# Performance work log

Measured on AMD Instinct MI355X. Metric: run time of the kernel, lower is better.

## Reference

```python
import jax, jax.numpy as jnp
import numpy as np

B, D = 8192, 128          # batch, input_dim (one graph node per feature)
ENC1, ENC2 = 256, 128     # encoder hidden dims (encoder_l = 3)
DEC1, DEC2 = 64, 32       # GCN decoder feature dims (decoder_l = 2)
THRESH = 0.1              # adjacency threshold after iter > 50


def setup_inputs():
    key = jax.random.key(0)
    ks = jax.random.split(key, 10)
    f32 = jnp.float32

    def w(k, shape, scale=0.05):
        return jax.random.normal(k, shape, f32) * scale

    return {
        "x": jax.random.normal(ks[0], (B, D), f32),
        "eps": jax.random.normal(ks[1], (B, D), f32),
        "W_enc1": w(ks[2], (D, ENC1)), "b_enc1": jnp.zeros((ENC1,), f32),
        "W_enc2": w(ks[3], (ENC1, ENC2)), "b_enc2": jnp.zeros((ENC2,), f32),
        "W_mu": w(ks[4], (ENC2, D)), "b_mu": jnp.zeros((D,), f32),
        "W_lv": w(ks[5], (ENC2, D)), "b_lv": jnp.zeros((D,), f32),
        "graph_logits": jax.random.normal(ks[6], (D, D), f32),
        "W_feat": w(ks[7], (1, DEC1), 0.1),
        "W_g1": w(ks[8], (DEC1, DEC2)), "b_g1": jnp.zeros((DEC2,), f32),
        "W_g2": w(ks[9], (DEC2, 1)), "b_g2": jnp.zeros((1,), f32),
        "it": 100,
    }


def _learned_graph(graph_logits, it):
    g = jax.nn.sigmoid(graph_logits)
    eye = jnp.eye(g.shape[0], dtype=g.dtype)
    g = g * (1.0 - eye) + eye                 # force self-loops to weight 1
    if it > 50:                               # static python int -> plain if
        g = jnp.where(g < THRESH, jnp.zeros_like(g), g)
    return g


def _gcn(adj, h, W, b):
    # DGL GraphConv norm='both' with edge weights on a batch of identical
    # D-node graphs (block-diagonal batching done densely per-sample):
    #   h' = D_in^{-1/2} (A_w)^T D_out^{-1/2} h W + b
    mask = (adj > 0).astype(h.dtype)
    d_out = jnp.maximum(mask.sum(axis=1), 1.0)
    d_in = jnp.maximum(mask.sum(axis=0), 1.0)
    a_hat = adj * jax.lax.rsqrt(d_out)[:, None] * jax.lax.rsqrt(d_in)[None, :]
    msg = jnp.einsum("ij,bif->bjf", a_hat, h)  # aggregate src->dst over all batch graphs
    return msg @ W + b


def reference(x, eps, W_enc1, b_enc1, W_enc2, b_enc2, W_mu, b_mu, W_lv, b_lv,
              graph_logits, W_feat, W_g1, b_g1, W_g2, b_g2, it):
    # --- VAE encoder + reparameterize ---
    h = jax.nn.relu(x @ W_enc1 + b_enc1)
    h = jax.nn.relu(h @ W_enc2 + b_enc2)
    mu_z = h @ W_mu + b_mu
    logvar_z = h @ W_lv + b_lv
    z = mu_z + eps * jnp.exp(0.5 * logvar_z)   # (B, D)
    # --- learned adjacency over features ---
    adj = _learned_graph(graph_logits, it)     # (D, D)
    # --- graph input processor: each feature -> one node, embed its scalar ---
    hn = z[:, :, None] * W_feat[0]             # (B, D, DEC1)
    # --- homogeneous GCN decoder ---
    hn = jnp.tanh(_gcn(adj, hn, W_g1, b_g1))   # (B, D, DEC2)
    hn = _gcn(adj, hn, W_g2, b_g2)             # (B, D, 1)
    x_hat = hn.reshape(x.shape[0], -1)         # (B, D)
    return (x_hat, adj, mu_z, logvar_z)
```

## Files before the change

### kernel.cpp

```cpp
#include <hip/hip_runtime.h>
#include <math.h>

#define BATCH 8192
#define DIM   128
#define E1    256
#define E2    128

#define OUT_XHAT 0
#define OUT_ADJ  (BATCH*DIM)
#define OUT_MU   (OUT_ADJ + DIM*DIM)
#define OUT_LV   (OUT_MU + BATCH*DIM)

#define W1F   0u
#define W2F   65536u
#define WMUF  131072u
#define WLVF  163840u
#define AHF   196608u
#define COEF  229376u
#define VBUF  229408u

typedef __attribute__((ext_vector_type(8))) short s8v;
typedef __attribute__((ext_vector_type(4))) float f4v;
#define MFMA(a, b, c) __builtin_amdgcn_mfma_f32_16x16x32_bf16(a, b, c, 0, 0, 0)

__device__ __forceinline__ ushort f2bf(float f) {
    uint u = __float_as_uint(f);
    u += 0x7fffu + ((u >> 16) & 1u);
    return (ushort)(u >> 16);
}

__global__ __launch_bounds__(512) void prep_kernel(
    const float* __restrict__ W1,  const float* __restrict__ W2,
    const float* __restrict__ Wmu, const float* __restrict__ Wlv,
    const float* __restrict__ logits, const float* __restrict__ Wf,
    const float* __restrict__ Wg1, const float* __restrict__ bg1,
    const float* __restrict__ Wg2, const int* __restrict__ itp,
    float* __restrict__ out, char* __restrict__ wsb)
{
    __shared__ float gsm[16384];
    __shared__ float aux[768];
    __shared__ float vsh[32];
    const int t = threadIdx.x;

    if (blockIdx.x < 24) {
        const int tid = (int)blockIdx.x * 512 + t;
        const float* W; ushort* dst; int e, N_, ksLog;
        if (tid < 4096)       { W = W1;  dst = (ushort*)(wsb + W1F);  e = tid * 8;           N_ = 256; ksLog = 2; }
        else if (tid < 8192)  { W = W2;  dst = (ushort*)(wsb + W2F);  e = (tid - 4096) * 8;  N_ = 128; ksLog = 3; }
        else if (tid < 10240) { W = Wmu; dst = (ushort*)(wsb + WMUF); e = (tid - 8192) * 8;  N_ = 128; ksLog = 2; }
        else                  { W = Wlv; dst = (ushort*)(wsb + WLVF); e = (tid - 10240) * 8; N_ = 128; ksLog = 2; }
        const int frag = e >> 9, l = (e >> 3) & 63;
        const int nt = frag >> ksLog, ks = frag & ((1 << ksLog) - 1);
        const int k0 = ks * 32 + ((l >> 4) << 3);
        const int n  = (nt << 4) + (l & 15);
        uint pk[4];
        #pragma unroll
        for (int jj = 0; jj < 4; ++jj) {
            ushort lo = f2bf(W[(k0 + 2 * jj) * N_ + n]);
            ushort hi = f2bf(W[(k0 + 2 * jj + 1) * N_ + n]);
            pk[jj] = (uint)lo | ((uint)hi << 16);
        }
        *(uint4*)(dst + e) = make_uint4(pk[0], pk[1], pk[2], pk[3]);
        return;
    }

    const int it = itp[0];
    {
        const int j = t & 127, rq = t >> 7;
        float dp = 0.0f;
        for (int i = rq * 32; i < rq * 32 + 32; ++i) {
            float l = logits[i * DIM + j];
            float gv = 1.0f / (1.0f + expf(-l));
            if (i == j) gv = 1.0f;
            if (it > 50 && gv < 0.1f) gv = 0.0f;
            gsm[i * DIM + j] = gv;
            if (gv > 0.0f) dp += 1.0f;
        }
        aux[rq * 128 + j] = dp;
    }
    __syncthreads();
    if (t < 128) {
        float d = aux[t] + aux[128 + t] + aux[256 + t] + aux[384 + t];
        aux[512 + t] = 1.0f / sqrtf(fmaxf(d, 1.0f));
    }
    __syncthreads();
    {
        const int i = t & 127, cq = t >> 7;
        float dp = 0.0f;
        for (int c = cq * 32; c < cq * 32 + 32; ++c)
            if (gsm[i * DIM + c] > 0.0f) dp += 1.0f;
        aux[cq * 128 + i] = dp;
    }
    __syncthreads();
    if (t < 128) {
        float d = aux[t] + aux[128 + t] + aux[256 + t] + aux[384 + t];
        aux[640 + t] = 1.0f / sqrtf(fmaxf(d, 1.0f));
    }
    __syncthreads();
    for (int p = 0; p < 32; ++p) {
        int idx = t + 512 * p;
        int i = idx >> 7, j = idx & 127;
        float gv = gsm[idx];
        out[OUT_ADJ + idx] = gv;
        gsm[idx] = gv * aux[640 + i] * aux[512 + j];
    }
    if (t < 32) {
        float acc = 0.0f;
        for (int k = 0; k < 64; ++k) acc = fmaf(Wf[k], Wg1[k * 32 + t], acc);
        vsh[t] = acc;
        float* vb = (float*)(wsb + VBUF);
        vb[t] = acc; vb[32 + t] = bg1[t]; vb[64 + t] = Wg2[t];
    }
    __syncthreads();
    {
        ushort* ahf = (ushort*)(wsb + AHF);
        #pragma unroll
        for (int c = 0; c < 4; ++c) {
            int e = (t + c * 512) * 8;
            int frag = e >> 9, l = (e >> 3) & 63;
            int nt = frag >> 2, ks = frag & 3;
            int k0 = ks * 32 + ((l >> 4) << 3);
            int n  = (nt << 4) + (l & 15);
            uint pk[4];
            #pragma unroll
            for (int jj = 0; jj < 4; ++jj) {
                ushort lo = f2bf(gsm[(k0 + 2 * jj) * DIM + n]);
                ushort hi = f2bf(gsm[(k0 + 2 * jj + 1) * DIM + n]);
                pk[jj] = (uint)lo | ((uint)hi << 16);
            }
            *(uint4*)(ahf + e) = make_uint4(pk[0], pk[1], pk[2], pk[3]);
        }
    }
    if (t == 0) {
        float a1 = 0, a3 = 0, a5 = 0, vmax = 0, bmax = 0;
        for (int c = 0; c < 32; ++c) {
            float v = vsh[c], w = Wg2[c], v2 = v * v;
            a1 += w * v;
            a3 -= w * v * v2 * (1.0f / 3.0f);
            a5 += w * v * v2 * v2 * (2.0f / 15.0f);
            vmax = fmaxf(vmax, fabsf(v));
            bmax = fmaxf(bmax, fabsf(bg1[c]));
        }
        float* cf = (float*)(wsb + COEF);
        cf[0] = a1; cf[1] = a3; cf[2] = a5;
        cf[3] = (bmax == 0.0f) ? 0.2f / fmaxf(vmax, 1e-30f) : -1.0f;
    }
}

__global__ __launch_bounds__(256, 2) void fused_kernel(
    const float* __restrict__ x,   const float* __restrict__ eps,
    const float* __restrict__ b1,  const float* __restrict__ b2,
    const float* __restrict__ bmu, const float* __restrict__ blv,
    const float* __restrict__ bg2p,
    float* __restrict__ out, char* __restrict__ wsb)
{
    __shared__ __attribute__((aligned(16))) ushort bufA[2048];
    __shared__ __attribute__((aligned(16))) ushort bufB[4096];
    __shared__ __attribute__((aligned(16))) ushort bufC[2048];
    __shared__ float vls[96];

    const int t = threadIdx.x;
    const int lane = t & 63, wid = t >> 6;
    const int fr = lane & 15, fq = lane >> 4;
    const int row0 = (int)blockIdx.x * 16;

    if (t < 96) vls[t] = ((const float*)(wsb + VBUF))[t];

    {
        const int r = t & 15, g = (t >> 4) & 3, ks = t >> 6;
        const float* src = x + (size_t)(row0 + r) * DIM + ks * 32 + g * 8;
        float4 u0 = *(const float4*)src;
        float4 u1 = *(const float4*)(src + 4);
        uint p0 = (uint)f2bf(u0.x) | ((uint)f2bf(u0.y) << 16);
        uint p1 = (uint)f2bf(u0.z) | ((uint)f2bf(u0.w) << 16);
        uint p2 = (uint)f2bf(u1.x) | ((uint)f2bf(u1.y) << 16);
        uint p3 = (uint)f2bf(u1.z) | ((uint)f2bf(u1.w) << 16);
        *(uint4*)&bufA[(ks * 64 + g * 16 + r) * 8] = make_uint4(p0, p1, p2, p3);
    }
    __syncthreads();

    {
        const ushort* w1f = (const ushort*)(wsb + W1F);
        f4v acc[4] = {{0,0,0,0},{0,0,0,0},{0,0,0,0},{0,0,0,0}};
        #pragma unroll
        for (int ks = 0; ks < 4; ++ks) {
            s8v a = *(const s8v*)&bufA[(ks * 64 + lane) * 8];
            #pragma unroll
            for (int n = 0; n < 4; ++n) {
                s8v b = *(const s8v*)&w1f[(((wid * 4 + n) * 4 + ks) * 64 + lane) * 8];
                acc[n] = MFMA(a, b, acc[n]);
            }
        }
        __syncthreads();
        #pragma unroll
        for (int n = 0; n < 4; ++n) {
            int col = wid * 64 + n * 16 + fr;
            float bb = b1[col];
            int base = (col >> 5) * 512 + (((col >> 3) & 3) * 16) * 8 + (col & 7);
            #pragma unroll
            for (int q = 0; q < 4; ++q)
                bufB[base + (fq * 4 + q) * 8] = f2bf(fmaxf(acc[n][q] + bb, 0.0f));
        }
    }
    __syncthreads();

    {
        const ushort* w2f = (const ushort*)(wsb + W2F);
        f4v acc[2] = {{0,0,0,0},{0,0,0,0}};
        #pragma unroll
        for (int ks = 0; ks < 8; ++ks) {
            s8v a = *(const s8v*)&bufB[(ks * 64 + lane) * 8];
            #pragma unroll
            for (int n = 0; n < 2; ++n) {
                s8v b = *(const s8v*)&w2f[(((wid * 2 + n) * 8 + ks) * 64 + lane) * 8];
                acc[n] = MFMA(a, b, acc[n]);
            }
        }
        #pragma unroll
        for (int n = 0; n < 2; ++n) {
            int col = wid * 32 + n * 16 + fr;
            float bb = b2[col];
            int base = (col >> 5) * 512 + (((col >> 3) & 3) * 16) * 8 + (col & 7);
            #pragma unroll
            for (int q = 0; q < 4; ++q)
                bufC[base + (fq * 4 + q) * 8] = f2bf(fmaxf(acc[n][q] + bb, 0.0f));
        }
    }
    __syncthreads();

    {
        const ushort* wmf = (const ushort*)(wsb + WMUF);
        const ushort* wlf = (const ushort*)(wsb + WLVF);
        f4v am[2] = {{0,0,0,0},{0,0,0,0}}, al[2] = {{0,0,0,0},{0,0,0,0}};
        #pragma unroll
        for (int ks = 0; ks < 4; ++ks) {
            s8v a = *(const s8v*)&bufC[(ks * 64 + lane) * 8];
            #pragma unroll
            for (int n = 0; n < 2; ++n) {
                int fi = (((wid * 2 + n) * 4 + ks) * 64 + lane) * 8;
                s8v bm = *(const s8v*)&wmf[fi];
                s8v bl = *(const s8v*)&wlf[fi];
                am[n] = MFMA(a, bm, am[n]);
                al[n] = MFMA(a, bl, al[n]);
            }
        }
        #pragma unroll
        for (int n = 0; n < 2; ++n) {
            int col = wid * 32 + n * 16 + fr;
            float bm = bmu[col], bl = blv[col];
            int base = (col >> 5) * 512 + (((col >> 3) & 3) * 16) * 8 + (col & 7);
            #pragma unroll
            for (int q = 0; q < 4; ++q) {
                int grow = row0 + fq * 4 + q;
                float mu = am[n][q] + bm;
                float lv = al[n][q] + bl;
                out[OUT_MU + grow * DIM + col] = mu;
                out[OUT_LV + grow * DIM + col] = lv;
                float z = fmaf(eps[grow * DIM + col], __expf(0.5f * lv), mu);
                bufA[base + (fq * 4 + q) * 8] = f2bf(z);
            }
        }
    }
    __syncthreads();

    const ushort* ahf = (const ushort*)(wsb + AHF);
    const float* cf = (const float*)(wsb + COEF);
    const float a1 = cf[0], a3 = cf[1], a5 = cf[2], ssafe = cf[3];

    s8v bfr[2][4];
    #pragma unroll
    for (int n = 0; n < 2; ++n)
        #pragma unroll
        for (int ks = 0; ks < 4; ++ks)
            bfr[n][ks] = *(const s8v*)&ahf[(((wid * 2 + n) * 4 + ks) * 64 + lane) * 8];

    f4v sa[2] = {{0,0,0,0},{0,0,0,0}};
    #pragma unroll
    for (int ks = 0; ks < 4; ++ks) {
        s8v a = *(const s8v*)&bufA[(ks * 64 + lane) * 8];
        sa[0] = MFMA(a, bfr[0][ks], sa[0]);
        sa[1] = MFMA(a, bfr[1][ks], sa[1]);
    }
    __syncthreads();

    #pragma unroll
    for (int n = 0; n < 2; ++n) {
        int k2 = wid * 32 + n * 16 + fr;
        int base = (k2 >> 5) * 512 + (((k2 >> 3) & 3) * 16) * 8 + (k2 & 7);
        #pragma unroll
        for (int q = 0; q < 4; ++q) {
            float s = sa[n][q];
            float tv;
            if (fabsf(s) < ssafe) {
                float s2 = s * s;
                tv = s * fmaf(s2, fmaf(s2, a5, a3), a1);
            } else {
                tv = 0.0f;
                for (int c = 0; c < 32; ++c)
                    tv = fmaf(vls[64 + c], tanhf(fmaf(s, vls[c], vls[32 + c])), tv);
            }
            bufB[base + (fq * 4 + q) * 8] = f2bf(tv);
        }
    }
    __syncthreads();

    f4v xa[2] = {{0,0,0,0},{0,0,0,0}};
    #pragma unroll
    for (int ks = 0; ks < 4; ++ks) {
        s8v a = *(const s8v*)&bufB[(ks * 64 + lane) * 8];
        xa[0] = MFMA(a, bfr[0][ks], xa[0]);
        xa[1] = MFMA(a, bfr[1][ks], xa[1]);
    }
    const float bg2v = bg2p[0];
    #pragma unroll
    for (int n = 0; n < 2; ++n) {
        int col = wid * 32 + n * 16 + fr;
        #pragma unroll
        for (int q = 0; q < 4; ++q)
            out[OUT_XHAT + (size_t)(row0 + fq * 4 + q) * DIM + col] = xa[n][q] + bg2v;
    }
}

extern "C" void kernel_launch(void* const* d_in, const int* in_sizes, int n_in,
                              void* d_out, int out_size, void* d_ws, size_t ws_size,
                              hipStream_t stream)
{
    const float* x      = (const float*)d_in[0];
    const float* eps    = (const float*)d_in[1];
    const float* W1     = (const float*)d_in[2];
    const float* b1     = (const float*)d_in[3];
    const float* W2     = (const float*)d_in[4];
    const float* b2     = (const float*)d_in[5];
    const float* Wmu    = (const float*)d_in[6];
    const float* bmu    = (const float*)d_in[7];
    const float* Wlv    = (const float*)d_in[8];
    const float* blv    = (const float*)d_in[9];
    const float* logits = (const float*)d_in[10];
    const float* Wf     = (const float*)d_in[11];
    const float* Wg1    = (const float*)d_in[12];
    const float* bg1    = (const float*)d_in[13];
    const float* Wg2    = (const float*)d_in[14];
    const float* bg2    = (const float*)d_in[15];
    const int*   itp    = (const int*)d_in[16];
    float* out = (float*)d_out;
    char* wsb  = (char*)d_ws;

    hipLaunchKernelGGL(prep_kernel, dim3(25), dim3(512), 0, stream,
                       W1, W2, Wmu, Wlv, logits, Wf, Wg1, bg1, Wg2, itp, out, wsb);
    hipLaunchKernelGGL(fused_kernel, dim3(BATCH / 16), dim3(256), 0, stream,
                       x, eps, b1, b2, bmu, blv, bg2, out, wsb);
}
```

Measured before the change: 26.28 us.

## Process 32 rows per block with 8 waves sharing each weight fragment

Each block now handles 32 batch rows with 512 threads (8 waves). Every wave loads one weight B-fragment and reuses it for two row tiles, which halves global weight-fragment traffic per output. The eps values are prefetched into registers at kernel start, so that global load overlaps the encoder GEMMs. In exchange, the grid is half as large (256 blocks), shared memory per block doubles, and launch bounds drop to one block per CU, which may reduce latency hiding.

```diff
diff --git a/kernel.cpp b/kernel.cpp
--- a/kernel.cpp
+++ b/kernel.cpp
@@ -5,6 +5,7 @@
 #define DIM   128
 #define E1    256
 #define E2    128
+#define BRF   32
 
 #define OUT_XHAT 0
 #define OUT_ADJ  (BATCH*DIM)
@@ -147,27 +148,37 @@
     }
 }
 
-__global__ __launch_bounds__(256, 2) void fused_kernel(
+__global__ __launch_bounds__(512, 1) void fused_kernel(
     const float* __restrict__ x,   const float* __restrict__ eps,
     const float* __restrict__ b1,  const float* __restrict__ b2,
     const float* __restrict__ bmu, const float* __restrict__ blv,
     const float* __restrict__ bg2p,
     float* __restrict__ out, char* __restrict__ wsb)
 {
-    __shared__ __attribute__((aligned(16))) ushort bufA[2048];
-    __shared__ __attribute__((aligned(16))) ushort bufB[4096];
-    __shared__ __attribute__((aligned(16))) ushort bufC[2048];
+    __shared__ __attribute__((aligned(16))) ushort bufA[4096];
+    __shared__ __attribute__((aligned(16))) ushort bufB[8192];
+    __shared__ __attribute__((aligned(16))) ushort bufC[4096];
     __shared__ float vls[96];
 
     const int t = threadIdx.x;
     const int lane = t & 63, wid = t >> 6;
     const int fr = lane & 15, fq = lane >> 4;
-    const int row0 = (int)blockIdx.x * 16;
+    const int row0 = (int)blockIdx.x * BRF;
+
+    float epr[2][4];
+    {
+        const float* eb = eps + (size_t)(row0 + fq * 4) * DIM + wid * 16 + fr;
+        #pragma unroll
+        for (int mt = 0; mt < 2; ++mt)
+            #pragma unroll
+            for (int q = 0; q < 4; ++q)
+                epr[mt][q] = eb[(mt * 16 + q) * DIM];
+    }
 
     if (t < 96) vls[t] = ((const float*)(wsb + VBUF))[t];
 
     {
-        const int r = t & 15, g = (t >> 4) & 3, ks = t >> 6;
+        const int r = t & 31, g = (t >> 5) & 3, ks = t >> 7;
         const float* src = x + (size_t)(row0 + r) * DIM + ks * 32 + g * 8;
         float4 u0 = *(const float4*)src;
         float4 u1 = *(const float4*)(src + 4);
@@ -175,31 +186,36 @@
         uint p1 = (uint)f2bf(u0.z) | ((uint)f2bf(u0.w) << 16);
         uint p2 = (uint)f2bf(u1.x) | ((uint)f2bf(u1.y) << 16);
         uint p3 = (uint)f2bf(u1.z) | ((uint)f2bf(u1.w) << 16);
-        *(uint4*)&bufA[(ks * 64 + g * 16 + r) * 8] = make_uint4(p0, p1, p2, p3);
+        *(uint4*)&bufA[(((r >> 4) * 4 + ks) * 64 + g * 16 + (r & 15)) * 8] =
+            make_uint4(p0, p1, p2, p3);
     }
     __syncthreads();
 
     {
         const ushort* w1f = (const ushort*)(wsb + W1F);
-        f4v acc[4] = {{0,0,0,0},{0,0,0,0},{0,0,0,0},{0,0,0,0}};
+        f4v acc[2][2] = {{{0,0,0,0},{0,0,0,0}},{{0,0,0,0},{0,0,0,0}}};
         #pragma unroll
         for (int ks = 0; ks < 4; ++ks) {
-            s8v a = *(const s8v*)&bufA[(ks * 64 + lane) * 8];
-            #pragma unroll
-            for (int n = 0; n < 4; ++n) {
-                s8v b = *(const s8v*)&w1f[(((wid * 4 + n) * 4 + ks) * 64 + lane) * 8];
-                acc[n] = MFMA(a, b, acc[n]);
-            }
-        }
-        __syncthreads();
-        #pragma unroll
-        for (int n = 0; n < 4; ++n) {
-            int col = wid * 64 + n * 16 + fr;
+            s8v a0 = *(const s8v*)&bufA[((0 * 4 + ks) * 64 + lane) * 8];
+            s8v a1 = *(const s8v*)&bufA[((1 * 4 + ks) * 64 + lane) * 8];
+            #pragma unroll
+            for (int n = 0; n < 2; ++n) {
+                s8v b = *(const s8v*)&w1f[(((2 * wid + n) * 4 + ks) * 64 + lane) * 8];
+                acc[0][n] = MFMA(a0, b, acc[0][n]);
+                acc[1][n] = MFMA(a1, b, acc[1][n]);
+            }
+        }
+        #pragma unroll
+        for (int n = 0; n < 2; ++n) {
+            int col = (2 * wid + n) * 16 + fr;
             float bb = b1[col];
-            int base = (col >> 5) * 512 + (((col >> 3) & 3) * 16) * 8 + (col & 7);
-            #pragma unroll
-            for (int q = 0; q < 4; ++q)
-                bufB[base + (fq * 4 + q) * 8] = f2bf(fmaxf(acc[n][q] + bb, 0.0f));
+            #pragma unroll
+            for (int mt = 0; mt < 2; ++mt) {
+                int base = ((mt * 8 + (col >> 5)) * 64 + ((col >> 3) & 3) * 16) * 8 + (col & 7);
+                #pragma unroll
+                for (int q = 0; q < 4; ++q)
+                    bufB[base + (fq * 4 + q) * 8] = f2bf(fmaxf(acc[mt][n][q] + bb, 0.0f));
+            }
         }
     }
     __syncthreads();
@@ -209,21 +225,20 @@
         f4v acc[2] = {{0,0,0,0},{0,0,0,0}};
         #pragma unroll
         for (int ks = 0; ks < 8; ++ks) {
-            s8v a = *(const s8v*)&bufB[(ks * 64 + lane) * 8];
-            #pragma unroll
-            for (int n = 0; n < 2; ++n) {
-                s8v b = *(const s8v*)&w2f[(((wid * 2 + n) * 8 + ks) * 64 + lane) * 8];
-                acc[n] = MFMA(a, b, acc[n]);
-            }
-        }
-        #pragma unroll
-        for (int n = 0; n < 2; ++n) {
-            int col = wid * 32 + n * 16 + fr;
-            float bb = b2[col];
-            int base = (col >> 5) * 512 + (((col >> 3) & 3) * 16) * 8 + (col & 7);
+            s8v a0 = *(const s8v*)&bufB[((0 * 8 + ks) * 64 + lane) * 8];
+            s8v a1 = *(const s8v*)&bufB[((1 * 8 + ks) * 64 + lane) * 8];
+            s8v b  = *(const s8v*)&w2f[((wid * 8 + ks) * 64 + lane) * 8];
+            acc[0] = MFMA(a0, b, acc[0]);
+            acc[1] = MFMA(a1, b, acc[1]);
+        }
+        int col = wid * 16 + fr;
+        float bb = b2[col];
+        #pragma unroll
+        for (int mt = 0; mt < 2; ++mt) {
+            int base = ((mt * 4 + (col >> 5)) * 64 + ((col >> 3) & 3) * 16) * 8 + (col & 7);
             #pragma unroll
             for (int q = 0; q < 4; ++q)
-                bufC[base + (fq * 4 + q) * 8] = f2bf(fmaxf(acc[n][q] + bb, 0.0f));
+                bufC[base + (fq * 4 + q) * 8] = f2bf(fmaxf(acc[mt][q] + bb, 0.0f));
         }
     }
     __syncthreads();
@@ -234,29 +249,29 @@
         f4v am[2] = {{0,0,0,0},{0,0,0,0}}, al[2] = {{0,0,0,0},{0,0,0,0}};
         #pragma unroll
         for (int ks = 0; ks < 4; ++ks) {
-            s8v a = *(const s8v*)&bufC[(ks * 64 + lane) * 8];
-            #pragma unroll
-            for (int n = 0; n < 2; ++n) {
-                int fi = (((wid * 2 + n) * 4 + ks) * 64 + lane) * 8;
-                s8v bm = *(const s8v*)&wmf[fi];
-                s8v bl = *(const s8v*)&wlf[fi];
-                am[n] = MFMA(a, bm, am[n]);
-                al[n] = MFMA(a, bl, al[n]);
-            }
-        }
-        #pragma unroll
-        for (int n = 0; n < 2; ++n) {
-            int col = wid * 32 + n * 16 + fr;
-            float bm = bmu[col], bl = blv[col];
-            int base = (col >> 5) * 512 + (((col >> 3) & 3) * 16) * 8 + (col & 7);
+            s8v a0 = *(const s8v*)&bufC[((0 * 4 + ks) * 64 + lane) * 8];
+            s8v a1 = *(const s8v*)&bufC[((1 * 4 + ks) * 64 + lane) * 8];
+            int fi = ((wid * 4 + ks) * 64 + lane) * 8;
+            s8v bm = *(const s8v*)&wmf[fi];
+            s8v bl = *(const s8v*)&wlf[fi];
+            am[0] = MFMA(a0, bm, am[0]);
+            am[1] = MFMA(a1, bm, am[1]);
+            al[0] = MFMA(a0, bl, al[0]);
+            al[1] = MFMA(a1, bl, al[1]);
+        }
+        int col = wid * 16 + fr;
+        float bm = bmu[col], bl = blv[col];
+        #pragma unroll
+        for (int mt = 0; mt < 2; ++mt) {
+            int base = ((mt * 4 + (col >> 5)) * 64 + ((col >> 3) & 3) * 16) * 8 + (col & 7);
             #pragma unroll
             for (int q = 0; q < 4; ++q) {
-                int grow = row0 + fq * 4 + q;
-                float mu = am[n][q] + bm;
-                float lv = al[n][q] + bl;
+                int grow = row0 + mt * 16 + fq * 4 + q;
+                float mu = am[mt][q] + bm;
+                float lv = al[mt][q] + bl;
                 out[OUT_MU + grow * DIM + col] = mu;
                 out[OUT_LV + grow * DIM + col] = lv;
-                float z = fmaf(eps[grow * DIM + col], __expf(0.5f * lv), mu);
+                float z = fmaf(epr[mt][q], __expf(0.5f * lv), mu);
                 bufA[base + (fq * 4 + q) * 8] = f2bf(z);
             }
         }
@@ -267,39 +282,40 @@
     const float* cf = (const float*)(wsb + COEF);
     const float a1 = cf[0], a3 = cf[1], a5 = cf[2], ssafe = cf[3];
 
-    s8v bfr[2][4];
+    s8v bfr[4];
     #pragma unroll
-    for (int n = 0; n < 2; ++n)
-        #pragma unroll
-        for (int ks = 0; ks < 4; ++ks)
-            bfr[n][ks] = *(const s8v*)&ahf[(((wid * 2 + n) * 4 + ks) * 64 + lane) * 8];
+    for (int ks = 0; ks < 4; ++ks)
+        bfr[ks] = *(const s8v*)&ahf[((wid * 4 + ks) * 64 + lane) * 8];
 
     f4v sa[2] = {{0,0,0,0},{0,0,0,0}};
     #pragma unroll
     for (int ks = 0; ks < 4; ++ks) {
-        s8v a = *(const s8v*)&bufA[(ks * 64 + lane) * 8];
-        sa[0] = MFMA(a, bfr[0][ks], sa[0]);
-        sa[1] = MFMA(a, bfr[1][ks], sa[1]);
-    }
-    __syncthreads();
-
-    #pragma unroll
-    for (int n = 0; n < 2; ++n) {
-        int k2 = wid * 32 + n * 16 + fr;
-        int base = (k2 >> 5) * 512 + (((k2 >> 3) & 3) * 16) * 8 + (k2 & 7);
-        #pragma unroll
-        for (int q = 0; q < 4; ++q) {
-            float s = sa[n][q];
-            float tv;
-            if (fabsf(s) < ssafe) {
-                float s2 = s * s;
-                tv = s * fmaf(s2, fmaf(s2, a5, a3), a1);
-            } else {
-                tv = 0.0f;
-                for (int c = 0; c < 32; ++c)
-                    tv = fmaf(vls[64 + c], tanhf(fmaf(s, vls[c], vls[32 + c])), tv);
-            }
-            bufB[base + (fq * 4 + q) * 8] = f2bf(tv);
+        s8v a0 = *(const s8v*)&bufA[((0 * 4 + ks) * 64 + lane) * 8];
+        s8v a1 = *(const s8v*)&bufA[((1 * 4 + ks) * 64 + lane) * 8];
+        sa[0] = MFMA(a0, bfr[ks], sa[0]);
+        sa[1] = MFMA(a1, bfr[ks], sa[1]);
+    }
+    __syncthreads();
+
+    {
+        int col = wid * 16 + fr;
+        #pragma unroll
+        for (int mt = 0; mt < 2; ++mt) {
+            int base = ((mt * 4 + (col >> 5)) * 64 + ((col >> 3) & 3) * 16) * 8 + (col & 7);
+            #pragma unroll
+            for (int q = 0; q < 4; ++q) {
+                float s = sa[mt][q];
+                float tv;
+                if (fabsf(s) < ssafe) {
+                    float s2 = s * s;
+                    tv = s * fmaf(s2, fmaf(s2, a5, a3), a1);
+                } else {
+                    tv = 0.0f;
+                    for (int c = 0; c < 32; ++c)
+                        tv = fmaf(vls[64 + c], tanhf(fmaf(s, vls[c], vls[32 + c])), tv);
+                }
+                bufB[base + (fq * 4 + q) * 8] = f2bf(tv);
+            }
         }
     }
     __syncthreads();
@@ -307,17 +323,20 @@
     f4v xa[2] = {{0,0,0,0},{0,0,0,0}};
     #pragma unroll
     for (int ks = 0; ks < 4; ++ks) {
-        s8v a = *(const s8v*)&bufB[(ks * 64 + lane) * 8];
-        xa[0] = MFMA(a, bfr[0][ks], xa[0]);
-        xa[1] = MFMA(a, bfr[1][ks], xa[1]);
+        s8v a0 = *(const s8v*)&bufB[((0 * 4 + ks) * 64 + lane) * 8];
+        s8v a1 = *(const s8v*)&bufB[((1 * 4 + ks) * 64 + lane) * 8];
+        xa[0] = MFMA(a0, bfr[ks], xa[0]);
+        xa[1] = MFMA(a1, bfr[ks], xa[1]);
     }
     const float bg2v = bg2p[0];
-    #pragma unroll
-    for (int n = 0; n < 2; ++n) {
-        int col = wid * 32 + n * 16 + fr;
-        #pragma unroll
-        for (int q = 0; q < 4; ++q)
-            out[OUT_XHAT + (size_t)(row0 + fq * 4 + q) * DIM + col] = xa[n][q] + bg2v;
+    {
+        int col = wid * 16 + fr;
+        #pragma unroll
+        for (int mt = 0; mt < 2; ++mt)
+            #pragma unroll
+            for (int q = 0; q < 4; ++q)
+                out[OUT_XHAT + (size_t)(row0 + mt * 16 + fq * 4 + q) * DIM + col] =
+                    xa[mt][q] + bg2v;
     }
 }
 
@@ -347,6 +366,6 @@
 
     hipLaunchKernelGGL(prep_kernel, dim3(25), dim3(512), 0, stream,
                        W1, W2, Wmu, Wlv, logits, Wf, Wg1, bg1, Wg2, itp, out, wsb);
-    hipLaunchKernelGGL(fused_kernel, dim3(BATCH / 16), dim3(256), 0, stream,
+    hipLaunchKernelGGL(fused_kernel, dim3(BATCH / BRF), dim3(512), 0, stream,
                        x, eps, b1, b2, bmu, blv, bg2, out, wsb);
 }
```

Result: faster. 25.50 us (-3.0%).

## Use 8 waves per block with one 16-column tile per wave, prefetch eps

Applied to the files above, without the earlier changes.

Doubles the fused kernel block to 512 threads, so each of 8 wavefronts owns a single 16-column MFMA tile per stage instead of two or four. This cuts per-wave serial MFMA chains and register use, and aims for more waves in flight per CU to hide latency. The eps values are also loaded into registers at kernel start so the global read overlaps the encoder GEMMs. In exchange there are more threads per block sharing the same barriers, and the x staging now uses narrower 8-byte loads.

```diff
diff --git a/kernel.cpp b/kernel.cpp
--- a/kernel.cpp
+++ b/kernel.cpp
@@ -5,6 +5,7 @@
 #define DIM   128
 #define E1    256
 #define E2    128
+#define BRF   16
 
 #define OUT_XHAT 0
 #define OUT_ADJ  (BATCH*DIM)
@@ -147,7 +148,7 @@
     }
 }
 
-__global__ __launch_bounds__(256, 2) void fused_kernel(
+__global__ __launch_bounds__(512, 4) void fused_kernel(
     const float* __restrict__ x,   const float* __restrict__ eps,
     const float* __restrict__ b1,  const float* __restrict__ b2,
     const float* __restrict__ bmu, const float* __restrict__ blv,
@@ -162,39 +163,44 @@
     const int t = threadIdx.x;
     const int lane = t & 63, wid = t >> 6;
     const int fr = lane & 15, fq = lane >> 4;
-    const int row0 = (int)blockIdx.x * 16;
+    const int row0 = (int)blockIdx.x * BRF;
+
+    float epr[4];
+    {
+        const float* eb = eps + (size_t)(row0 + fq * 4) * DIM + wid * 16 + fr;
+        #pragma unroll
+        for (int q = 0; q < 4; ++q) epr[q] = eb[q * DIM];
+    }
 
     if (t < 96) vls[t] = ((const float*)(wsb + VBUF))[t];
 
     {
-        const int r = t & 15, g = (t >> 4) & 3, ks = t >> 6;
-        const float* src = x + (size_t)(row0 + r) * DIM + ks * 32 + g * 8;
-        float4 u0 = *(const float4*)src;
-        float4 u1 = *(const float4*)(src + 4);
-        uint p0 = (uint)f2bf(u0.x) | ((uint)f2bf(u0.y) << 16);
-        uint p1 = (uint)f2bf(u0.z) | ((uint)f2bf(u0.w) << 16);
-        uint p2 = (uint)f2bf(u1.x) | ((uint)f2bf(u1.y) << 16);
-        uint p3 = (uint)f2bf(u1.z) | ((uint)f2bf(u1.w) << 16);
-        *(uint4*)&bufA[(ks * 64 + g * 16 + r) * 8] = make_uint4(p0, p1, p2, p3);
+        const int r = t & 15, c16 = t >> 4;
+        const int k0 = c16 * 4;
+        const int ks = k0 >> 5, g = (k0 & 31) >> 3, h = (k0 >> 2) & 1;
+        float4 u = *(const float4*)(x + (size_t)(row0 + r) * DIM + k0);
+        uint p0 = (uint)f2bf(u.x) | ((uint)f2bf(u.y) << 16);
+        uint p1 = (uint)f2bf(u.z) | ((uint)f2bf(u.w) << 16);
+        *(uint2*)&bufA[(ks * 64 + g * 16 + r) * 8 + h * 4] = make_uint2(p0, p1);
     }
     __syncthreads();
 
     {
         const ushort* w1f = (const ushort*)(wsb + W1F);
-        f4v acc[4] = {{0,0,0,0},{0,0,0,0},{0,0,0,0},{0,0,0,0}};
+        f4v acc[2] = {{0,0,0,0},{0,0,0,0}};
         #pragma unroll
         for (int ks = 0; ks < 4; ++ks) {
             s8v a = *(const s8v*)&bufA[(ks * 64 + lane) * 8];
             #pragma unroll
-            for (int n = 0; n < 4; ++n) {
-                s8v b = *(const s8v*)&w1f[(((wid * 4 + n) * 4 + ks) * 64 + lane) * 8];
+            for (int n = 0; n < 2; ++n) {
+                s8v b = *(const s8v*)&w1f[(((2 * wid + n) * 4 + ks) * 64 + lane) * 8];
                 acc[n] = MFMA(a, b, acc[n]);
             }
         }
         __syncthreads();
         #pragma unroll
-        for (int n = 0; n < 4; ++n) {
-            int col = wid * 64 + n * 16 + fr;
+        for (int n = 0; n < 2; ++n) {
+            int col = (2 * wid + n) * 16 + fr;
             float bb = b1[col];
             int base = (col >> 5) * 512 + (((col >> 3) & 3) * 16) * 8 + (col & 7);
             #pragma unroll
@@ -206,59 +212,47 @@
 
     {
         const ushort* w2f = (const ushort*)(wsb + W2F);
-        f4v acc[2] = {{0,0,0,0},{0,0,0,0}};
+        f4v acc = {0, 0, 0, 0};
         #pragma unroll
         for (int ks = 0; ks < 8; ++ks) {
             s8v a = *(const s8v*)&bufB[(ks * 64 + lane) * 8];
-            #pragma unroll
-            for (int n = 0; n < 2; ++n) {
-                s8v b = *(const s8v*)&w2f[(((wid * 2 + n) * 8 + ks) * 64 + lane) * 8];
-                acc[n] = MFMA(a, b, acc[n]);
-            }
-        }
-        #pragma unroll
-        for (int n = 0; n < 2; ++n) {
-            int col = wid * 32 + n * 16 + fr;
-            float bb = b2[col];
-            int base = (col >> 5) * 512 + (((col >> 3) & 3) * 16) * 8 + (col & 7);
-            #pragma unroll
-            for (int q = 0; q < 4; ++q)
-                bufC[base + (fq * 4 + q) * 8] = f2bf(fmaxf(acc[n][q] + bb, 0.0f));
-        }
+            s8v b = *(const s8v*)&w2f[((wid * 8 + ks) * 64 + lane) * 8];
+            acc = MFMA(a, b, acc);
+        }
+        int col = wid * 16 + fr;
+        float bb = b2[col];
+        int base = (col >> 5) * 512 + (((col >> 3) & 3) * 16) * 8 + (col & 7);
+        #pragma unroll
+        for (int q = 0; q < 4; ++q)
+            bufC[base + (fq * 4 + q) * 8] = f2bf(fmaxf(acc[q] + bb, 0.0f));
     }
     __syncthreads();
 
     {
         const ushort* wmf = (const ushort*)(wsb + WMUF);
         const ushort* wlf = (const ushort*)(wsb + WLVF);
-        f4v am[2] = {{0,0,0,0},{0,0,0,0}}, al[2] = {{0,0,0,0},{0,0,0,0}};
+        f4v am = {0, 0, 0, 0}, al = {0, 0, 0, 0};
         #pragma unroll
         for (int ks = 0; ks < 4; ++ks) {
             s8v a = *(const s8v*)&bufC[(ks * 64 + lane) * 8];
-            #pragma unroll
-            for (int n = 0; n < 2; ++n) {
-                int fi = (((wid * 2 + n) * 4 + ks) * 64 + lane) * 8;
-                s8v bm = *(const s8v*)&wmf[fi];
-                s8v bl = *(const s8v*)&wlf[fi];
-                am[n] = MFMA(a, bm, am[n]);
-                al[n] = MFMA(a, bl, al[n]);
-            }
-        }
-        #pragma unroll
-        for (int n = 0; n < 2; ++n) {
-            int col = wid * 32 + n * 16 + fr;
-            float bm = bmu[col], bl = blv[col];
-            int base = (col >> 5) * 512 + (((col >> 3) & 3) * 16) * 8 + (col & 7);
-            #pragma unroll
-            for (int q = 0; q < 4; ++q) {
-                int grow = row0 + fq * 4 + q;
-                float mu = am[n][q] + bm;
-                float lv = al[n][q] + bl;
-                out[OUT_MU + grow * DIM + col] = mu;
-                out[OUT_LV + grow * DIM + col] = lv;
-                float z = fmaf(eps[grow * DIM + col], __expf(0.5f * lv), mu);
-                bufA[base + (fq * 4 + q) * 8] = f2bf(z);
-            }
+            int fi = ((wid * 4 + ks) * 64 + lane) * 8;
+            s8v bm = *(const s8v*)&wmf[fi];
+            s8v bl = *(const s8v*)&wlf[fi];
+            am = MFMA(a, bm, am);
+            al = MFMA(a, bl, al);
+        }
+        int col = wid * 16 + fr;
+        float bm = bmu[col], bl = blv[col];
+        int base = (col >> 5) * 512 + (((col >> 3) & 3) * 16) * 8 + (col & 7);
+        #pragma unroll
+        for (int q = 0; q < 4; ++q) {
+            int grow = row0 + fq * 4 + q;
+            float mu = am[q] + bm;
+            float lv = al[q] + bl;
+            out[OUT_MU + grow * DIM + col] = mu;
+            out[OUT_LV + grow * DIM + col] = lv;
+            float z = fmaf(epr[q], __expf(0.5f * lv), mu);
+            bufA[base + (fq * 4 + q) * 8] = f2bf(z);
         }
     }
     __syncthreads();
@@ -266,30 +260,26 @@
     const ushort* ahf = (const ushort*)(wsb + AHF);
     const float* cf = (const float*)(wsb + COEF);
     const float a1 = cf[0], a3 = cf[1], a5 = cf[2], ssafe = cf[3];
-
-    s8v bfr[2][4];
+    const int acol = wid * 16 + fr;
+
+    s8v bfr[4];
     #pragma unroll
-    for (int n = 0; n < 2; ++n)
-        #pragma unroll
-        for (int ks = 0; ks < 4; ++ks)
-            bfr[n][ks] = *(const s8v*)&ahf[(((wid * 2 + n) * 4 + ks) * 64 + lane) * 8];
-
-    f4v sa[2] = {{0,0,0,0},{0,0,0,0}};
+    for (int ks = 0; ks < 4; ++ks)
+        bfr[ks] = *(const s8v*)&ahf[((wid * 4 + ks) * 64 + lane) * 8];
+
+    f4v sa = {0, 0, 0, 0};
     #pragma unroll
     for (int ks = 0; ks < 4; ++ks) {
         s8v a = *(const s8v*)&bufA[(ks * 64 + lane) * 8];
-        sa[0] = MFMA(a, bfr[0][ks], sa[0]);
-        sa[1] = MFMA(a, bfr[1][ks], sa[1]);
-    }
-    __syncthreads();
-
-    #pragma unroll
-    for (int n = 0; n < 2; ++n) {
-        int k2 = wid * 32 + n * 16 + fr;
-        int base = (k2 >> 5) * 512 + (((k2 >> 3) & 3) * 16) * 8 + (k2 & 7);
+        sa = MFMA(a, bfr[ks], sa);
+    }
+    __syncthreads();
+
+    {
+        int base = (acol >> 5) * 512 + (((acol >> 3) & 3) * 16) * 8 + (acol & 7);
         #pragma unroll
         for (int q = 0; q < 4; ++q) {
-            float s = sa[n][q];
+            float s = sa[q];
             float tv;
             if (fabsf(s) < ssafe) {
                 float s2 = s * s;
@@ -304,21 +294,16 @@
     }
     __syncthreads();
 
-    f4v xa[2] = {{0,0,0,0},{0,0,0,0}};
+    f4v xa = {0, 0, 0, 0};
     #pragma unroll
     for (int ks = 0; ks < 4; ++ks) {
         s8v a = *(const s8v*)&bufB[(ks * 64 + lane) * 8];
-        xa[0] = MFMA(a, bfr[0][ks], xa[0]);
-        xa[1] = MFMA(a, bfr[1][ks], xa[1]);
+        xa = MFMA(a, bfr[ks], xa);
     }
     const float bg2v = bg2p[0];
     #pragma unroll
-    for (int n = 0; n < 2; ++n) {
-        int col = wid * 32 + n * 16 + fr;
-        #pragma unroll
-        for (int q = 0; q < 4; ++q)
-            out[OUT_XHAT + (size_t)(row0 + fq * 4 + q) * DIM + col] = xa[n][q] + bg2v;
-    }
+    for (int q = 0; q < 4; ++q)
+        out[OUT_XHAT + (size_t)(row0 + fq * 4 + q) * DIM + acol] = xa[q] + bg2v;
 }
 
 extern "C" void kernel_launch(void* const* d_in, const int* in_sizes, int n_in,
@@ -347,6 +332,6 @@
 
     hipLaunchKernelGGL(prep_kernel, dim3(25), dim3(512), 0, stream,
                        W1, W2, Wmu, Wlv, logits, Wf, Wg1, bg1, Wg2, itp, out, wsb);
-    hipLaunchKernelGGL(fused_kernel, dim3(BATCH / 16), dim3(256), 0, stream,
+    hipLaunchKernelGGL(fused_kernel, dim3(BATCH / BRF), dim3(512), 0, stream,
                        x, eps, b1, b2, bmu, blv, bg2, out, wsb);
 }
```

New measurement: 25.38 us. 3.4% less time.
